# Optimization experiments

Measured on AMD Instinct MI355X. Metric: run time of the kernel, lower is better.

Reference implementation:

```python
import jax, jax.numpy as jnp
import numpy as np

B, STATE_DIM, MLP_DIM, H, W = 128, 64, 512, 40, 40
LN_EPS = 1e-5


def _sobel_kernel(c):
    # Per-channel depthwise filters in torch order: [c0_sx, c0_sy, c0_id, c1_sx, ...]
    sx = jnp.array([[-1., 0., 1.], [-2., 0., 2.], [-1., 0., 1.]], jnp.float32)
    sy = jnp.array([[-1., -2., -1.], [0., 0., 0.], [1., 2., 1.]], jnp.float32)
    ident = jnp.array([[0., 0., 0.], [0., 1., 0.], [0., 0., 0.]], jnp.float32)
    k = jnp.stack([sx, sy, ident])[:, None]      # [3, 1, 3, 3]
    return jnp.tile(k, (c, 1, 1, 1))             # [3c, 1, 3, 3]


def setup_inputs() -> dict:
    key = jax.random.key(0)
    ks = jax.random.split(key, 6)
    state_in = jax.random.normal(ks[0], (B, STATE_DIM, H, W), jnp.float32)
    w1 = jax.random.normal(ks[1], (MLP_DIM, 3 * STATE_DIM), jnp.float32) * 0.05
    ln_weight = jax.random.uniform(ks[2], (MLP_DIM, H, W), jnp.float32, 0.5, 1.5)
    ln_bias = jax.random.normal(ks[3], (MLP_DIM, H, W), jnp.float32) * 0.01
    w2 = jax.random.normal(ks[4], (STATE_DIM, MLP_DIM), jnp.float32) * 0.05
    mask = jax.random.randint(ks[5], (H, W), 0, 2, jnp.int32)  # bernoulli(0.5) update mask
    return {"state_in": state_in, "w1": w1, "ln_weight": ln_weight,
            "ln_bias": ln_bias, "w2": w2, "mask": mask}


def reference(state_in, w1, ln_weight, ln_bias, w2, mask):
    C = state_in.shape[1]
    # Depthwise 3x3 sobel/identity perception: [B, C, H, W] -> [B, 3C, H, W]
    kern = _sobel_kernel(C)
    x = jax.lax.conv_general_dilated(
        state_in, kern, window_strides=(1, 1), padding='SAME',
        dimension_numbers=('NCHW', 'OIHW', 'NCHW'), feature_group_count=C)
    # 1x1 conv (no bias): [B, 3C, H, W] -> [B, MLP, H, W]
    x = jnp.einsum('bchw,oc->bohw', x, w1)
    # LayerNorm over (MLP, H, W) per sample, with elementwise affine
    mu = jnp.mean(x, axis=(1, 2, 3), keepdims=True)
    var = jnp.var(x, axis=(1, 2, 3), keepdims=True)
    x = (x - mu) * jax.lax.rsqrt(var + LN_EPS) * ln_weight + ln_bias
    x = jax.nn.relu(x)
    # 1x1 conv back to state channels (zero-init in original; random here for testing)
    x = jnp.einsum('bchw,oc->bohw', x, w2)
    # Stochastic per-pixel update mask, broadcast over batch and channels
    x = x * mask.astype(jnp.float32)
    # Alive mask: 3x3 max-pool on alive channel, stride 1, SAME padding
    live = jax.lax.reduce_window(state_in[:, 3], -jnp.inf, jax.lax.max,
                                 (1, 3, 3), (1, 1, 1), 'SAME')
    live = (live > 0.1).astype(jnp.float32)[:, None]  # [B, 1, H, W]
    return state_in + x * live
```

## Files before the change

### kernel.cpp

```cpp
#include <hip/hip_runtime.h>


typedef unsigned short u16;
typedef unsigned int   u32;
typedef __attribute__((ext_vector_type(8))) u16    ushort8;
typedef __attribute__((ext_vector_type(4))) u16    u16x4;
typedef __attribute__((ext_vector_type(8))) __bf16 bf16x8;
typedef __attribute__((ext_vector_type(4))) float  f32x4;
typedef __attribute__((ext_vector_type(4))) u32    u32x4;

#define NB   128
#define NC   64
#define K1   192
#define NO   512
#define NHW  1600
#define LN_N 819200.0f

__device__ __forceinline__ u16 f2bf(float f) {
    union { float f; u32 u; } v; v.f = f;
    u32 u = v.u;
    u32 r = u + 0x7fffu + ((u >> 16) & 1u);
    return (u16)(r >> 16);
}
__device__ __forceinline__ float bf2f(u16 h) {
    union { u32 u; float f; } v; v.u = ((u32)h) << 16; return v.f;
}
__device__ __forceinline__ float bfhi(u32 c) {
    union { u32 u; float f; } v; v.u = c & 0xffff0000u; return v.f;
}
__device__ __forceinline__ float bflo(u32 c) {
    union { u32 u; float f; } v; v.u = c << 16; return v.f;
}
__device__ __forceinline__ f32x4 mfma16(bf16x8 a, bf16x8 b, f32x4 c) {
    return __builtin_amdgcn_mfma_f32_16x16x32_bf16(a, b, c, 0, 0, 0);
}
__device__ __forceinline__ bf16x8 ldfrag(const u16* p) {
    return *(const bf16x8*)p;
}

__device__ __forceinline__ void load_halo(const float* __restrict__ base, int h,
                                          int wq, float reg[3][12]) {
#pragma unroll
    for (int jj = 0; jj < 3; ++jj) {
        int hh = h + jj - 1;
        bool vh = (unsigned)hh < 40u;
        const float* rowp = base + hh * 40;
#pragma unroll
        for (int i = 0; i < 12; ++i) {
            int col = wq * 10 - 1 + i;
            reg[jj][i] = (vh && (unsigned)col < 40u) ? rowp[col] : 0.0f;
        }
    }
}
__device__ __forceinline__ void sobel_px(const float reg[3][12], int t,
                                         float& sx, float& sy, float& idn) {
    sx = (reg[0][t + 2] - reg[0][t]) + 2.0f * (reg[1][t + 2] - reg[1][t])
       + (reg[2][t + 2] - reg[2][t]);
    sy = (reg[2][t] + 2.0f * reg[2][t + 1] + reg[2][t + 2])
       - (reg[0][t] + 2.0f * reg[0][t + 1] + reg[0][t + 2]);
    idn = reg[1][t + 1];
}

__global__ __launch_bounds__(256) void k0_convert(const float* __restrict__ w1,
                                                  const float* __restrict__ w2,
                                                  u16* __restrict__ w1p,
                                                  u16* __restrict__ w1T,
                                                  u16* __restrict__ w2p,
                                                  float* __restrict__ stats) {
    int g = blockIdx.x * 256 + threadIdx.x;
    if (g < NO * K1) {
        u16 v = f2bf(w1[g]);
        int o = g / K1, k = g - o * K1;
        int f = o >> 4, ks = k >> 5;
        int lane = (((k >> 3) & 3) << 4) | (o & 15);
        w1p[(size_t)(((f * 6 + ks) * 64 + lane) * 8 + (k & 7))] = v;
        w1T[(size_t)k * NO + o] = v;
    } else if (g < NO * K1 + NC * NO) {
        int i = g - NO * K1;
        int s = i / NO, o = i - s * NO;
        u16 v = f2bf(w2[i]);
        int wid = s >> 4, oc = o >> 6, ks2 = (o >> 5) & 1;
        int lane = (((o >> 3) & 3) << 4) | (s & 15);
        w2p[(size_t)((((wid * 8 + oc) * 2 + ks2) * 64 + lane) * 8 + (o & 7))] = v;
    } else if (g < NO * K1 + NC * NO + 256) {
        stats[g - NO * K1 - NC * NO] = 0.0f;
    }
}

__global__ __launch_bounds__(256) void k0_lncomb(const float* __restrict__ lnw,
                                                 const float* __restrict__ lnb,
                                                 u32* __restrict__ lnp) {
    int g = blockIdx.x * 256 + threadIdx.x;
    int r = g & 3;
    int lane = (g >> 2) & 63;
    int rest = g >> 8;
    int mi = rest % 5;  rest /= 5;
    int wid = rest & 3; rest >>= 2;
    int oc = rest & 7;
    int bx = rest >> 3;
    int p = bx * 80 + mi * 16 + (lane & 15);
    int o = oc * 64 + wid * 16 + ((lane >> 4) << 2) + r;
    size_t gi = (size_t)o * NHW + p;
    lnp[g] = ((u32)f2bf(lnb[gi]) << 16) | f2bf(lnw[gi]);
}

__global__ __launch_bounds__(256) void k0_gram(const u16* __restrict__ w1T,
                                               float* __restrict__ G,
                                               float* __restrict__ colw1) {
    const int blk = blockIdx.x;
    const int tid = threadIdx.x;
    const int lane = tid & 63, wid = tid >> 6;
    const int q = lane >> 4, l15 = lane & 15;
    if (blk < 36) {
        int bj = blk / 6, bk = blk - bj * 6;
        int j0 = bj * 32 + (wid & 1) * 16, k0 = bk * 32 + (wid >> 1) * 16;
        f32x4 acc = {0.f, 0.f, 0.f, 0.f};
#pragma unroll
        for (int ks = 0; ks < 16; ++ks) {
            bf16x8 a  = ldfrag(&w1T[(size_t)(j0 + l15) * NO + ks * 32 + q * 8]);
            bf16x8 bb = ldfrag(&w1T[(size_t)(k0 + l15) * NO + ks * 32 + q * 8]);
            acc = mfma16(a, bb, acc);
        }
#pragma unroll
        for (int r = 0; r < 4; ++r)
            G[(size_t)(j0 + q * 4 + r) * K1 + k0 + l15] = acc[r];
    } else if (tid < K1) {
        float s = 0.f;
        for (int i = 0; i < NO / 8; ++i) {
            ushort8 v = *(const ushort8*)&w1T[(size_t)tid * NO + i * 8];
#pragma unroll
            for (int j = 0; j < 8; ++j) s += bf2f(v[j]);
        }
        colw1[tid] = s;
    }
}

__global__ __launch_bounds__(256) void k2_stats(const float* __restrict__ state,
                                                const float* __restrict__ G,
                                                const float* __restrict__ colw1,
                                                float* __restrict__ stats) {
    const int b = blockIdx.x >> 2, quarter = blockIdx.x & 3;
    const int tid = threadIdx.x;
    const int lane = tid & 63, wid = tid >> 6;
    const int q = lane >> 4, l15 = lane & 15;
    const int j0 = (wid & 1) * 96, j1 = (wid >> 1) * 96, jo = wid * 48;

    __shared__ __align__(16) u16 Pt[208 * 104];
    __shared__ float red[8];

    for (int i = tid; i < 208 * 104 / 2; i += 256) ((u32*)Pt)[i] = 0u;
    __syncthreads();
    if (tid < 80) Pt[192 * 104 + tid] = 0x3F80u;

    f32x4 acc[6][6], accO[3];
#pragma unroll
    for (int i = 0; i < 6; ++i)
#pragma unroll
        for (int j = 0; j < 6; ++j) { f32x4 z = {0.f,0.f,0.f,0.f}; acc[i][j] = z; }
#pragma unroll
    for (int j = 0; j < 3; ++j) { f32x4 z = {0.f,0.f,0.f,0.f}; accO[j] = z; }

    const int c = tid >> 2, wq = tid & 3;
    const float* base = state + ((size_t)b * NC + c) * NHW;

    for (int tile = 0; tile < 5; ++tile) {
        const int h0 = (quarter * 5 + tile) * 2;
        __syncthreads();
        for (int rr = 0; rr < 2; ++rr) {
            float reg[3][12];
            load_halo(base, h0 + rr, wq, reg);
#pragma unroll
            for (int t = 0; t < 10; ++t) {
                float sx, sy, idn; sobel_px(reg, t, sx, sy, idn);
                int px = rr * 40 + wq * 10 + t;
                Pt[(3 * c + 0) * 104 + px] = f2bf(sx);
                Pt[(3 * c + 1) * 104 + px] = f2bf(sy);
                Pt[(3 * c + 2) * 104 + px] = f2bf(idn);
            }
        }
        __syncthreads();
#pragma unroll
        for (int ks = 0; ks < 3; ++ks) {
            bf16x8 av[6], bv[6], ao, bo[3];
#pragma unroll
            for (int fi = 0; fi < 6; ++fi)
                av[fi] = ldfrag(&Pt[(j0 + fi * 16 + l15) * 104 + ks * 32 + q * 8]);
#pragma unroll
            for (int fj = 0; fj < 6; ++fj)
                bv[fj] = ldfrag(&Pt[(j1 + fj * 16 + l15) * 104 + ks * 32 + q * 8]);
            ao = ldfrag(&Pt[(192 + l15) * 104 + ks * 32 + q * 8]);
#pragma unroll
            for (int fj = 0; fj < 3; ++fj)
                bo[fj] = ldfrag(&Pt[(jo + fj * 16 + l15) * 104 + ks * 32 + q * 8]);
#pragma unroll
            for (int fi = 0; fi < 6; ++fi)
#pragma unroll
                for (int fj = 0; fj < 6; ++fj)
                    acc[fi][fj] = mfma16(av[fi], bv[fj], acc[fi][fj]);
#pragma unroll
            for (int fj = 0; fj < 3; ++fj)
                accO[fj] = mfma16(ao, bo[fj], accO[fj]);
        }
    }

    float ssq = 0.f;
#pragma unroll
    for (int fi = 0; fi < 6; ++fi)
#pragma unroll
        for (int fj = 0; fj < 6; ++fj) {
            f32x4 gv = *(const f32x4*)&G[(size_t)(j1 + fj * 16 + l15) * K1
                                         + j0 + fi * 16 + q * 4];
#pragma unroll
            for (int r = 0; r < 4; ++r) ssq += acc[fi][fj][r] * gv[r];
        }
    float sm = 0.f;
    if (q == 0) {
#pragma unroll
        for (int fj = 0; fj < 3; ++fj)
            sm += accO[fj][0] * colw1[jo + fj * 16 + l15];
    }
#pragma unroll
    for (int off = 32; off > 0; off >>= 1) {
        ssq += __shfl_down(ssq, off);
        sm  += __shfl_down(sm, off);
    }
    if (lane == 0) { red[wid] = ssq; red[4 + wid] = sm; }
    __syncthreads();
    if (tid == 0) {
        atomicAdd(&stats[b * 2],     red[4] + red[5] + red[6] + red[7]);
        atomicAdd(&stats[b * 2 + 1], red[0] + red[1] + red[2] + red[3]);
    }
}

__global__ void k3_finalize(const float* __restrict__ stats, float2* __restrict__ musig) {
    int t = threadIdx.x;
    if (t < NB) {
        float s = stats[2 * t], qq = stats[2 * t + 1];
        float inv = 1.0f / LN_N;
        float mu = s * inv;
        float var = qq * inv - mu * mu;
        float2 r; r.x = mu; r.y = rsqrtf(var + 1e-5f);
        musig[t] = r;
    }
}

__global__ __launch_bounds__(256, 4) void k4_fused(const float* __restrict__ state,
                                                   const u16* __restrict__ w1p,
                                                   const u16* __restrict__ w2p,
                                                   const u32* __restrict__ lnp,
                                                   const int* __restrict__ mask,
                                                   const float2* __restrict__ musig,
                                                   float* __restrict__ out) {
    const int bx = blockIdx.x;
    const int b  = blockIdx.y;
    const int p0 = bx * 80, h0 = bx * 2;
    const int tid = threadIdx.x;
    const int lane = tid & 63, wid = tid >> 6;
    const int q = lane >> 4, l15 = lane & 15;

    __shared__ __align__(16) u16 Pt[80 * 192];
    __shared__ __align__(16) u16 Ys[80 * 64];

    const float2 ms = musig[b];
    const float mu = ms.x, rs = ms.y;
    const float murs = mu * rs;

    {
        const int c = tid >> 2, wq = tid & 3;
        const float* base = state + ((size_t)b * NC + c) * NHW;
        for (int rr = 0; rr < 2; ++rr) {
            float reg[3][12];
            load_halo(base, h0 + rr, wq, reg);
#pragma unroll
            for (int t = 0; t < 10; ++t) {
                float sx, sy, idn; sobel_px(reg, t, sx, sy, idn);
                int px = rr * 40 + wq * 10 + t;
                int k = 3 * c;
#pragma unroll
                for (int i = 0; i < 3; ++i) {
                    int kk = k + i, u = kk >> 3;
                    int elem = px * 192 + (((u & 0x18) | ((u ^ px) & 7)) << 3) + (kk & 7);
                    Pt[elem] = f2bf(i == 0 ? sx : (i == 1 ? sy : idn));
                }
            }
        }
    }
    float g5[5];
    {
        const float* st3 = state + ((size_t)b * NC + 3) * NHW;
#pragma unroll
        for (int mi = 0; mi < 5; ++mi) {
            int p = p0 + mi * 16 + l15;
            int h = p / 40, w = p - h * 40;
            float mx = -1e30f;
#pragma unroll
            for (int dh = -1; dh <= 1; ++dh) {
                int hh = h + dh;
                if ((unsigned)hh < 40u)
#pragma unroll
                    for (int dw = -1; dw <= 1; ++dw) {
                        int wc = w + dw;
                        if ((unsigned)wc < 40u) mx = fmaxf(mx, st3[hh * 40 + wc]);
                    }
            }
            g5[mi] = (mx > 0.1f && mask[p] != 0) ? 1.0f : 0.0f;
        }
    }
    __syncthreads();

    f32x4 acc2[5];
#pragma unroll
    for (int i = 0; i < 5; ++i) { f32x4 z = {0.f,0.f,0.f,0.f}; acc2[i] = z; }

    for (int oc = 0; oc < 8; ++oc) {
        u32x4 lv[5];
        {
            const u32* lb = lnp + ((((size_t)bx * 8 + oc) * 4 + wid) * 5) * 256 + lane * 4;
#pragma unroll
            for (int mi = 0; mi < 5; ++mi)
                lv[mi] = *(const u32x4*)(lb + mi * 256);
        }
        const u16* w2base = w2p + ((size_t)(wid * 8 + oc) * 2) * 512 + lane * 8;
        bf16x8 aw0 = ldfrag(w2base);
        bf16x8 aw1 = ldfrag(w2base + 512);

        f32x4 acc1[5];
#pragma unroll
        for (int i = 0; i < 5; ++i) { f32x4 z = {0.f,0.f,0.f,0.f}; acc1[i] = z; }
        const u16* w1base = w1p + ((size_t)(oc * 4 + wid) * 6) * 512 + lane * 8;
#pragma unroll
        for (int ks = 0; ks < 6; ++ks) {
            bf16x8 a = ldfrag(w1base + ks * 512);
#pragma unroll
            for (int mi = 0; mi < 5; ++mi) {
                int r = mi * 16 + l15, u = ks * 4 + q;
                bf16x8 bp = ldfrag(&Pt[r * 192 + (((u & 0x18) | ((u ^ r) & 7)) << 3)]);
                acc1[mi] = mfma16(a, bp, acc1[mi]);
            }
        }
#pragma unroll
        for (int mi = 0; mi < 5; ++mi) {
            int p = mi * 16 + l15;
            u16x4 yv;
#pragma unroll
            for (int r = 0; r < 4; ++r) {
                u32 cc = lv[mi][r];
                float t = fmaf(acc1[mi][r], rs, -murs);
                float y = fmaf(t, bflo(cc), bfhi(cc));
                yv[r] = f2bf(fmaxf(y, 0.0f));
            }
            int u = wid * 2 + (q >> 1);
            int up = u ^ (p & 7);
            *(u16x4*)&Ys[p * 64 + up * 8 + (q & 1) * 4] = yv;
        }
        __syncthreads();
#pragma unroll
        for (int ks2 = 0; ks2 < 2; ++ks2) {
            bf16x8 aw = ks2 ? aw1 : aw0;
#pragma unroll
            for (int mi = 0; mi < 5; ++mi) {
                int p = mi * 16 + l15;
                int u = ks2 * 4 + q;
                int up = u ^ (p & 7);
                bf16x8 by = ldfrag(&Ys[p * 64 + up * 8]);
                acc2[mi] = mfma16(aw, by, acc2[mi]);
            }
        }
        __syncthreads();
    }

#pragma unroll
    for (int mi = 0; mi < 5; ++mi) {
        int p = p0 + mi * 16 + l15;
        float g = g5[mi];
#pragma unroll
        for (int r = 0; r < 4; ++r) {
            int s = wid * 16 + q * 4 + r;
            size_t idx = ((size_t)b * NC + s) * NHW + p;
            out[idx] = state[idx] + g * acc2[mi][r];
        }
    }
}

extern "C" void kernel_launch(void* const* d_in, const int* in_sizes, int n_in,
                              void* d_out, int out_size, void* d_ws, size_t ws_size,
                              hipStream_t stream) {
    const float* state = (const float*)d_in[0];
    const float* w1    = (const float*)d_in[1];
    const float* lnw   = (const float*)d_in[2];
    const float* lnb   = (const float*)d_in[3];
    const float* w2    = (const float*)d_in[4];
    const int*   mask  = (const int*)d_in[5];
    float* out = (float*)d_out;

    char* ws = (char*)d_ws;
    u16*    w1p   = (u16*)(ws + 0ull);
    u16*    w2p   = (u16*)(ws + 196608ull);
    u32*    lnp   = (u32*)(ws + 262144ull);
    u16*    w1T   = (u16*)(ws + 3538944ull);
    float*  G     = (float*)(ws + 3735552ull);
    float*  colw1 = (float*)(ws + 3883008ull);
    float*  stats = (float*)(ws + 3883776ull);
    float2* musig = (float2*)(ws + 3884800ull);

    k0_convert <<<513, 256, 0, stream>>>(w1, w2, w1p, w1T, w2p, stats);
    k0_lncomb  <<<3200, 256, 0, stream>>>(lnw, lnb, lnp);
    k0_gram    <<<37, 256, 0, stream>>>(w1T, G, colw1);
    k2_stats   <<<512, 256, 0, stream>>>(state, G, colw1, stats);
    k3_finalize<<<1, 128, 0, stream>>>(stats, musig);
    k4_fused   <<<dim3(20, 128), 256, 0, stream>>>(state, w1p, w2p, lnp,
                                                   mask, musig, out);
}
```

Measured before the change: 303.4 us.

## Double-buffer Ys to drop a barrier, precompute swizzled LDS offsets, coalesce LN packing

Result: slower. 321.8 us (+6.1%).

```diff
diff --git a/kernel.cpp b/kernel.cpp
--- a/kernel.cpp
+++ b/kernel.cpp
@@ -17,10 +17,7 @@
 #define LN_N 819200.0f
 
 __device__ __forceinline__ u16 f2bf(float f) {
-    union { float f; u32 u; } v; v.f = f;
-    u32 u = v.u;
-    u32 r = u + 0x7fffu + ((u >> 16) & 1u);
-    return (u16)(r >> 16);
+    union { __bf16 h; u16 u; } v; v.h = (__bf16)f; return v.u;
 }
 __device__ __forceinline__ float bf2f(u16 h) {
     union { u32 u; float f; } v; v.u = ((u32)h) << 16; return v.f;
@@ -91,17 +88,14 @@
                                                  const float* __restrict__ lnb,
                                                  u32* __restrict__ lnp) {
     int g = blockIdx.x * 256 + threadIdx.x;
-    int r = g & 3;
-    int lane = (g >> 2) & 63;
-    int rest = g >> 8;
-    int mi = rest % 5;  rest /= 5;
-    int wid = rest & 3; rest >>= 2;
-    int oc = rest & 7;
-    int bx = rest >> 3;
-    int p = bx * 80 + mi * 16 + (lane & 15);
-    int o = oc * 64 + wid * 16 + ((lane >> 4) << 2) + r;
-    size_t gi = (size_t)o * NHW + p;
-    lnp[g] = ((u32)f2bf(lnb[gi]) << 16) | f2bf(lnw[gi]);
+    int o = g / NHW, p = g - o * NHW;
+    int bx = p / 80, pr = p - bx * 80;
+    int mi = pr >> 4, l15 = pr & 15;
+    int oc = o >> 6, ro = o & 63;
+    int wid = ro >> 4, hi = (ro >> 2) & 3, r = ro & 3;
+    int lane = (hi << 4) | l15;
+    int outi = ((((bx * 8 + oc) * 4 + wid) * 5 + mi) << 8) + lane * 4 + r;
+    lnp[outi] = ((u32)f2bf(lnb[g]) << 16) | f2bf(lnw[g]);
 }
 
 __global__ __launch_bounds__(256) void k0_gram(const u16* __restrict__ w1T,
@@ -148,7 +142,7 @@
     __shared__ __align__(16) u16 Pt[208 * 104];
     __shared__ float red[8];
 
-    for (int i = tid; i < 208 * 104 / 2; i += 256) ((u32*)Pt)[i] = 0u;
+    for (int i = tid; i < 208 * 104 / 8; i += 256) ((u32x4*)Pt)[i] = (u32x4){0,0,0,0};
     __syncthreads();
     if (tid < 80) Pt[192 * 104 + tid] = 0x3F80u;
 
@@ -244,7 +238,7 @@
     }
 }
 
-__global__ __launch_bounds__(256, 4) void k4_fused(const float* __restrict__ state,
+__global__ __launch_bounds__(256, 3) void k4_fused(const float* __restrict__ state,
                                                    const u16* __restrict__ w1p,
                                                    const u16* __restrict__ w2p,
                                                    const u32* __restrict__ lnp,
@@ -259,7 +253,8 @@
     const int q = lane >> 4, l15 = lane & 15;
 
     __shared__ __align__(16) u16 Pt[80 * 192];
-    __shared__ __align__(16) u16 Ys[80 * 64];
+    __shared__ __align__(16) u16 Ys0[80 * 64];
+    __shared__ __align__(16) u16 Ys1[80 * 64];
 
     const float2 ms = musig[b];
     const float mu = ms.x, rs = ms.y;
@@ -306,13 +301,30 @@
             g5[mi] = (mx > 0.1f && mask[p] != 0) ? 1.0f : 0.0f;
         }
     }
+
+    int pB0[5], pB1[5], yR0[5], yR1[5], yW[5];
+    {
+        const int q8 = q << 3;
+        const int wu = wid * 2 + (q >> 1);
+#pragma unroll
+        for (int mi = 0; mi < 5; ++mi) {
+            int r  = mi * 16 + l15;
+            int xr = (r & 7) << 3;
+            pB0[mi] = r * 192 + (q8 ^ xr);
+            pB1[mi] = r * 192 + ((q8 + 32) ^ xr);
+            int px = r & 7;
+            yR0[mi] = r * 64 + ((q ^ px) << 3);
+            yR1[mi] = r * 64 + (((q + 4) ^ px) << 3);
+            yW[mi]  = r * 64 + ((wu ^ px) << 3) + (q & 1) * 4;
+        }
+    }
     __syncthreads();
 
     f32x4 acc2[5];
 #pragma unroll
     for (int i = 0; i < 5; ++i) { f32x4 z = {0.f,0.f,0.f,0.f}; acc2[i] = z; }
 
-    for (int oc = 0; oc < 8; ++oc) {
+    auto oc_body = [&](int oc, u16* __restrict__ ys) {
         u32x4 lv[5];
         {
             const u32* lb = lnp + ((((size_t)bx * 8 + oc) * 4 + wid) * 5) * 256 + lane * 4;
@@ -333,25 +345,21 @@
             bf16x8 a = ldfrag(w1base + ks * 512);
 #pragma unroll
             for (int mi = 0; mi < 5; ++mi) {
-                int r = mi * 16 + l15, u = ks * 4 + q;
-                bf16x8 bp = ldfrag(&Pt[r * 192 + (((u & 0x18) | ((u ^ r) & 7)) << 3)]);
-                acc1[mi] = mfma16(a, bp, acc1[mi]);
+                int off = ((ks & 1) ? pB1[mi] : pB0[mi]) + (ks >> 1) * 64;
+                acc1[mi] = mfma16(a, ldfrag(&Pt[off]), acc1[mi]);
             }
         }
 #pragma unroll
         for (int mi = 0; mi < 5; ++mi) {
-            int p = mi * 16 + l15;
             u16x4 yv;
 #pragma unroll
             for (int r = 0; r < 4; ++r) {
                 u32 cc = lv[mi][r];
                 float t = fmaf(acc1[mi][r], rs, -murs);
-                float y = fmaf(t, bflo(cc), bfhi(cc));
-                yv[r] = f2bf(fmaxf(y, 0.0f));
-            }
-            int u = wid * 2 + (q >> 1);
-            int up = u ^ (p & 7);
-            *(u16x4*)&Ys[p * 64 + up * 8 + (q & 1) * 4] = yv;
+                float y = fmaxf(fmaf(t, bflo(cc), bfhi(cc)), 0.0f);
+                yv[r] = f2bf(y);
+            }
+            *(u16x4*)&ys[yW[mi]] = yv;
         }
         __syncthreads();
 #pragma unroll
@@ -359,14 +367,14 @@
             bf16x8 aw = ks2 ? aw1 : aw0;
 #pragma unroll
             for (int mi = 0; mi < 5; ++mi) {
-                int p = mi * 16 + l15;
-                int u = ks2 * 4 + q;
-                int up = u ^ (p & 7);
-                bf16x8 by = ldfrag(&Ys[p * 64 + up * 8]);
-                acc2[mi] = mfma16(aw, by, acc2[mi]);
-            }
-        }
-        __syncthreads();
+                int off = ks2 ? yR1[mi] : yR0[mi];
+                acc2[mi] = mfma16(aw, ldfrag(&ys[off]), acc2[mi]);
+            }
+        }
+    };
+    for (int oc = 0; oc < 8; oc += 2) {
+        oc_body(oc,     Ys0);
+        oc_body(oc + 1, Ys1);
     }
 
 #pragma unroll
```
